# Kernel optimization log

Hardware: AMD Instinct MI355X
Metric: run time of the kernel (lower is better)

## Reference

```python
import jax, jax.numpy as jnp
import numpy as np

N_NODES = 50000
N_EDGES = 800000
NUM_FEATS = 128
HIDDEN = 256
NUM_GRAPHS = 512
BN_EPS = 1e-5


def setup_inputs() -> dict:
    key = jax.random.key(0)
    ks = jax.random.split(key, 12)
    x = jax.random.normal(ks[0], (N_NODES, NUM_FEATS), dtype=jnp.float32)
    edge_index = jax.random.randint(ks[1], (2, N_EDGES), 0, N_NODES, dtype=jnp.int64)
    batch = jnp.sort(jax.random.randint(ks[2], (N_NODES,), 0, NUM_GRAPHS, dtype=jnp.int64))
    s1 = 1.0 / np.sqrt(NUM_FEATS)
    s2 = 1.0 / np.sqrt(HIDDEN)
    return {
        "x": x,
        "edge_index": edge_index,
        "batch": batch,
        "w1a": jax.random.normal(ks[3], (NUM_FEATS, HIDDEN), dtype=jnp.float32) * s1,
        "b1a": jnp.zeros((HIDDEN,), jnp.float32),
        "w2a": jax.random.normal(ks[4], (HIDDEN, HIDDEN), dtype=jnp.float32) * s2,
        "b2a": jnp.zeros((HIDDEN,), jnp.float32),
        "ga": jnp.ones((HIDDEN,), jnp.float32),
        "ba": jnp.zeros((HIDDEN,), jnp.float32),
        "w1s": jax.random.normal(ks[5], (2, HIDDEN, HIDDEN), dtype=jnp.float32) * s2,
        "b1s": jnp.zeros((2, HIDDEN), jnp.float32),
        "w2s": jax.random.normal(ks[6], (2, HIDDEN, HIDDEN), dtype=jnp.float32) * s2,
        "b2s": jnp.zeros((2, HIDDEN), jnp.float32),
        "gs": jnp.ones((2, HIDDEN), jnp.float32),
        "bs": jnp.zeros((2, HIDDEN), jnp.float32),
    }


def _gin_layer(h, src, dst, w1, b1, w2, b2, gamma, beta):
    # GIN aggregation: (1 + eps=0) * x + sum over in-neighbors
    agg = jax.ops.segment_sum(h[src], dst, num_segments=N_NODES)
    z = h + agg
    z = jax.nn.relu(z @ w1 + b1)
    z = jax.nn.relu(z @ w2 + b2)
    # BatchNorm1d (training mode: biased batch statistics over nodes)
    mu = jnp.mean(z, axis=0)
    var = jnp.var(z, axis=0)
    return gamma * (z - mu) * jax.lax.rsqrt(var + BN_EPS) + beta


def reference(x, edge_index, batch, w1a, b1a, w2a, b2a, ga, ba,
              w1s, b1s, w2s, b2s, gs, bs):
    src, dst = edge_index[0], edge_index[1]
    h = _gin_layer(x, src, dst, w1a, b1a, w2a, b2a, ga, ba)
    for i in range(w1s.shape[0]):
        h = _gin_layer(h, src, dst, w1s[i], b1s[i], w2s[i], b2s[i], gs[i], bs[i])
    # global_mean_pool over graph ids
    sums = jax.ops.segment_sum(h, batch, num_segments=NUM_GRAPHS)
    counts = jax.ops.segment_sum(jnp.ones((h.shape[0],), h.dtype), batch,
                                 num_segments=NUM_GRAPHS)
    return sums / jnp.maximum(counts, 1.0)[:, None]
```

## Files before the change

kernel.cpp:

```cpp
#include <hip/hip_runtime.h>
#include <cstdint>
#include <cstddef>


constexpr int N_NODES  = 50000;
constexpr int N_EDGES  = 800000;
constexpr int F_IN     = 128;
constexpr int HID      = 256;
constexpr int N_GRAPHS = 512;
constexpr float BN_EPS = 1e-5f;

constexpr int SCAN_CHUNK = 4096;
constexpr int SCAN_NB    = (N_NODES + SCAN_CHUNK - 1) / SCAN_CHUNK;

typedef unsigned short u16;
typedef u16 u16x2 __attribute__((ext_vector_type(2)));
typedef u16 u16x4 __attribute__((ext_vector_type(4)));
typedef u16 u16x8 __attribute__((ext_vector_type(8)));
typedef _Float16 f16;
typedef f16 f16x8 __attribute__((ext_vector_type(8)));
typedef float f32x4 __attribute__((ext_vector_type(4)));

__device__ __forceinline__ u16 f2h(float f) {
    _Float16 h = (_Float16)f;
    return __builtin_bit_cast(u16, h);
}
__device__ __forceinline__ float h2f(u16 h) {
    return (float)__builtin_bit_cast(_Float16, h);
}

__device__ __forceinline__ void gload16(const void* g, void* l) {
    __builtin_amdgcn_global_load_lds(
        (const __attribute__((address_space(1))) uint32_t*)g,
        (__attribute__((address_space(3))) uint32_t*)l, 16, 0, 0);
}

__global__ void f2h_k(const float* __restrict__ in, u16* __restrict__ outp, int n8) {
    int i = blockIdx.x * 256 + threadIdx.x;
    if (i >= n8) return;
    float4 a = reinterpret_cast<const float4*>(in)[i * 2];
    float4 b = reinterpret_cast<const float4*>(in)[i * 2 + 1];
    u16x8 v;
    v[0] = f2h(a.x); v[1] = f2h(a.y); v[2] = f2h(a.z); v[3] = f2h(a.w);
    v[4] = f2h(b.x); v[5] = f2h(b.y); v[6] = f2h(b.z); v[7] = f2h(b.w);
    reinterpret_cast<u16x8*>(outp)[i] = v;
}

__global__ void hist_k(const int* __restrict__ dst, int* __restrict__ deg) {
    int e = blockIdx.x * 256 + threadIdx.x;
    if (e < N_EDGES) atomicAdd(&deg[dst[e]], 1);
}

__global__ void scan_part1(const int* __restrict__ in, int* __restrict__ bsum) {
    __shared__ int sm[256];
    int t = threadIdx.x;
    int base = blockIdx.x * SCAN_CHUNK + t * 16;
    int s = 0;
#pragma unroll
    for (int j = 0; j < 16; j++) { int idx = base + j; s += (idx < N_NODES) ? in[idx] : 0; }
    sm[t] = s; __syncthreads();
    for (int off = 128; off > 0; off >>= 1) {
        if (t < off) sm[t] += sm[t + off];
        __syncthreads();
    }
    if (t == 0) bsum[blockIdx.x] = sm[0];
}

__global__ void scan_tops(int* __restrict__ bsum, int* __restrict__ rowptr) {
    if (threadIdx.x == 0 && blockIdx.x == 0) {
        int acc = 0;
        for (int i = 0; i < SCAN_NB; i++) { int v = bsum[i]; bsum[i] = acc; acc += v; }
        rowptr[N_NODES] = acc;
    }
}

__global__ void scan_final(const int* __restrict__ in, const int* __restrict__ bsum,
                           int* __restrict__ rowptr, int* __restrict__ cursor) {
    __shared__ int sm[256];
    int t = threadIdx.x;
    int base = blockIdx.x * SCAN_CHUNK + t * 16;
    int loc[16]; int s = 0;
#pragma unroll
    for (int j = 0; j < 16; j++) { int idx = base + j; loc[j] = s; s += (idx < N_NODES) ? in[idx] : 0; }
    sm[t] = s; __syncthreads();
    for (int off = 1; off < 256; off <<= 1) {
        int v = (t >= off) ? sm[t - off] : 0;
        __syncthreads();
        sm[t] += v;
        __syncthreads();
    }
    int excl = sm[t] - s + bsum[blockIdx.x];
#pragma unroll
    for (int j = 0; j < 16; j++) {
        int idx = base + j;
        if (idx < N_NODES) { int rp = excl + loc[j]; rowptr[idx] = rp; cursor[idx] = rp; }
    }
}

__global__ void build_csr(const int* __restrict__ src, const int* __restrict__ dst,
                          int* __restrict__ cursor, int* __restrict__ col) {
    int e = blockIdx.x * 256 + threadIdx.x;
    if (e < N_EDGES) {
        int d = dst[e];
        int p = atomicAdd(&cursor[d], 1);
        col[p] = src[e];
    }
}

template <int F, bool FOLD>
__global__ __launch_bounds__(256) void aggregate_k(const u16* __restrict__ h,
                                                   const int* __restrict__ rowptr,
                                                   const int* __restrict__ col,
                                                   const float* __restrict__ stats,
                                                   const float* __restrict__ gamma,
                                                   const float* __restrict__ beta,
                                                   u16* __restrict__ outp) {
    int node = blockIdx.x * 4 + (threadIdx.x >> 6);
    if (node >= N_NODES) return;
    int lane = threadIdx.x & 63;
    int beg = rowptr[node], end = rowptr[node + 1];
    if constexpr (F == 256) {
        float sc[4], sh[4];
        if constexpr (FOLD) {
            int c4 = lane * 4;
#pragma unroll
            for (int i = 0; i < 4; i++) {
                float mu  = stats[c4 + i] * (1.f / N_NODES);
                float var = stats[HID + c4 + i] * (1.f / N_NODES) - mu * mu;
                float g = gamma[c4 + i] * rsqrtf(var + BN_EPS);
                sc[i] = g;
                sh[i] = beta[c4 + i] - mu * g;
            }
        }
        const u16x4* hp = reinterpret_cast<const u16x4*>(h);
        u16x4 sv = hp[(size_t)node * 64 + lane];
        float acc[4] = {h2f(sv[0]), h2f(sv[1]), h2f(sv[2]), h2f(sv[3])};
        int e = beg;
        for (; e + 4 <= end; e += 4) {
            int s0 = col[e], s1 = col[e + 1], s2 = col[e + 2], s3 = col[e + 3];
            u16x4 v0 = hp[(size_t)s0 * 64 + lane];
            u16x4 v1 = hp[(size_t)s1 * 64 + lane];
            u16x4 v2 = hp[(size_t)s2 * 64 + lane];
            u16x4 v3 = hp[(size_t)s3 * 64 + lane];
#pragma unroll
            for (int i = 0; i < 4; i++)
                acc[i] += (h2f(v0[i]) + h2f(v1[i])) + (h2f(v2[i]) + h2f(v3[i]));
        }
        for (; e < end; ++e) {
            int s = col[e];
            u16x4 v = hp[(size_t)s * 64 + lane];
#pragma unroll
            for (int i = 0; i < 4; i++) acc[i] += h2f(v[i]);
        }
        if constexpr (FOLD) {
            float m = (float)(end - beg + 1);
#pragma unroll
            for (int i = 0; i < 4; i++) acc[i] = acc[i] * sc[i] + m * sh[i];
        }
        u16x4 r;
#pragma unroll
        for (int i = 0; i < 4; i++) r[i] = f2h(acc[i]);
        reinterpret_cast<u16x4*>(outp)[(size_t)node * 64 + lane] = r;
    } else {
        const u16x2* hp = reinterpret_cast<const u16x2*>(h);
        u16x2 sv = hp[(size_t)node * 64 + lane];
        float acc[2] = {h2f(sv[0]), h2f(sv[1])};
        int e = beg;
        for (; e + 4 <= end; e += 4) {
            int s0 = col[e], s1 = col[e + 1], s2 = col[e + 2], s3 = col[e + 3];
            u16x2 v0 = hp[(size_t)s0 * 64 + lane];
            u16x2 v1 = hp[(size_t)s1 * 64 + lane];
            u16x2 v2 = hp[(size_t)s2 * 64 + lane];
            u16x2 v3 = hp[(size_t)s3 * 64 + lane];
#pragma unroll
            for (int i = 0; i < 2; i++)
                acc[i] += (h2f(v0[i]) + h2f(v1[i])) + (h2f(v2[i]) + h2f(v3[i]));
        }
        for (; e < end; ++e) {
            int s = col[e];
            u16x2 v = hp[(size_t)s * 64 + lane];
#pragma unroll
            for (int i = 0; i < 2; i++) acc[i] += h2f(v[i]);
        }
        u16x2 r;
        r[0] = f2h(acc[0]); r[1] = f2h(acc[1]);
        reinterpret_cast<u16x2*>(outp)[(size_t)node * 64 + lane] = r;
    }
}

__global__ void wconv_all(const float* __restrict__ w1a, const float* __restrict__ w2a,
                          const float* __restrict__ w1s, const float* __restrict__ w2s,
                          u16* __restrict__ th) {
    int idx = blockIdx.x * 256 + threadIdx.x;
    const float* W; int local; size_t dof;
    if (idx < 32768)       { W = w1a;         local = idx;          dof = 0; }
    else if (idx < 98304)  { W = w2a;         local = idx - 32768;  dof = 32768; }
    else if (idx < 163840) { W = w1s;         local = idx - 98304;  dof = 98304; }
    else if (idx < 229376) { W = w1s + 65536; local = idx - 163840; dof = 163840; }
    else if (idx < 294912) { W = w2s;         local = idx - 229376; dof = 229376; }
    else if (idx < 360448) { W = w2s + 65536; local = idx - 294912; dof = 294912; }
    else return;
    int n = local & 255, k = local >> 8;
    float f = W[(size_t)k * 256 + n];
    int t = k >> 5, j = (k >> 3) & 3, e = k & 7;
    int uo = j ^ ((n >> 1) & 3);
    th[dof + (size_t)t * 8192 + n * 32 + uo * 8 + e] = f2h(f);
}

template <int K, bool STATS>
__global__ __launch_bounds__(256, 2) void gemm_mfma(const u16* __restrict__ A,
                                                    const u16* __restrict__ Wth,
                                                    const float* __restrict__ bias,
                                                    u16* __restrict__ C,
                                                    float* __restrict__ stats) {
    constexpr int BM = 128, BK = 32;
    __shared__ alignas(16) u16 Ah[BM * BK];
    __shared__ alignas(16) u16 Bh[HID * BK];
    __shared__ float smsum[HID];
    __shared__ float smsq[HID];

    const int tid  = threadIdx.x;
    const int r0   = blockIdx.x * BM;
    const int lane = tid & 63, wv = tid >> 6;
    const int wm = wv >> 1, wn = wv & 1;
    const int l15 = lane & 15, kg = lane >> 4;

    int aro[2], aco[2];
#pragma unroll
    for (int p = 0; p < 2; p++) {
        int nu = wv * 128 + p * 64 + lane;
        int r = nu >> 2, us = nu & 3;
        int u = us ^ ((r >> 1) & 3);
        aro[p] = r;
        aco[p] = u * 8;
    }

    f32x4 acc[4][8];
#pragma unroll
    for (int i = 0; i < 4; i++)
#pragma unroll
        for (int j = 0; j < 8; j++) acc[i][j] = (f32x4){0.f, 0.f, 0.f, 0.f};

    for (int k0 = 0; k0 < K; k0 += BK) {
        int t = k0 >> 5;
#pragma unroll
        for (int p = 0; p < 2; p++) {
            const u16* src = A + (size_t)(r0 + aro[p]) * K + k0 + aco[p];
            gload16(src, (char*)Ah + (size_t)(wv * 2 + p) * 1024);
        }
        const char* wh = (const char*)Wth + (size_t)t * 16384 + (size_t)wv * 4096 + (size_t)lane * 16;
#pragma unroll
        for (int c = 0; c < 4; c++)
            gload16(wh + c * 1024, (char*)Bh + (size_t)wv * 4096 + c * 1024);
        __syncthreads();
        f16x8 ah[4];
#pragma unroll
        for (int mi = 0; mi < 4; mi++) {
            int r = wm * 64 + mi * 16 + l15;
            int off = r * 64 + ((kg ^ ((r >> 1) & 3)) << 4);
            ah[mi] = __builtin_bit_cast(f16x8, *reinterpret_cast<const u16x8*>((const char*)Ah + off));
        }
#pragma unroll
        for (int ni = 0; ni < 8; ni++) {
            int n = wn * 128 + ni * 16 + l15;
            int off = n * 64 + ((kg ^ ((n >> 1) & 3)) << 4);
            f16x8 bh = __builtin_bit_cast(f16x8, *reinterpret_cast<const u16x8*>((const char*)Bh + off));
#pragma unroll
            for (int mi = 0; mi < 4; mi++)
                acc[mi][ni] = __builtin_amdgcn_mfma_f32_16x16x32_f16(ah[mi], bh, acc[mi][ni], 0, 0, 0);
        }
        __syncthreads();
    }
    if constexpr (STATS) {
        smsum[tid] = 0.f;
        smsq[tid]  = 0.f;
        __syncthreads();
    }
    float bv[8];
#pragma unroll
    for (int ni = 0; ni < 8; ni++) bv[ni] = bias[wn * 128 + ni * 16 + l15];
    float ps[8] = {}, pq[8] = {};
#pragma unroll
    for (int mi = 0; mi < 4; mi++) {
        int rowb = r0 + wm * 64 + mi * 16 + kg * 4;
#pragma unroll
        for (int rr = 0; rr < 4; rr++) {
            int row = rowb + rr;
            if (row < N_NODES) {
                u16* cp = C + (size_t)row * HID + wn * 128 + l15;
#pragma unroll
                for (int ni = 0; ni < 8; ni++) {
                    float v = fmaxf(acc[mi][ni][rr] + bv[ni], 0.f);
                    cp[ni * 16] = f2h(v);
                    if constexpr (STATS) { ps[ni] += v; pq[ni] += v * v; }
                }
            }
        }
    }
    if constexpr (STATS) {
#pragma unroll
        for (int ni = 0; ni < 8; ni++) {
            int c = wn * 128 + ni * 16 + l15;
            atomicAdd(&smsum[c], ps[ni]);
            atomicAdd(&smsq[c], pq[ni]);
        }
        __syncthreads();
        atomicAdd(&stats[tid], smsum[tid]);
        atomicAdd(&stats[HID + tid], smsq[tid]);
    }
}

__device__ __forceinline__ int lowerb(const int* a, int key) {
    int lo = 0, hi = N_NODES;
    while (lo < hi) { int mid = (lo + hi) >> 1; if (a[mid] < key) lo = mid + 1; else hi = mid; }
    return lo;
}

__global__ void pool_k(const u16* __restrict__ h, const int* __restrict__ batch,
                       const float* __restrict__ stats, const float* __restrict__ gamma,
                       const float* __restrict__ beta, float* __restrict__ out) {
    __shared__ int bnd[2];
    int g = blockIdx.x;
    if (threadIdx.x == 0) bnd[0] = lowerb(batch, g);
    if (threadIdx.x == 1) bnd[1] = lowerb(batch, g + 1);
    __syncthreads();
    int lo = bnd[0], hi = bnd[1];
    int c = threadIdx.x;
    float mu  = stats[c] * (1.f / N_NODES);
    float var = stats[HID + c] * (1.f / N_NODES) - mu * mu;
    float sc = gamma[c] * rsqrtf(var + BN_EPS);
    float sh = beta[c] - mu * sc;
    float s = 0.f;
    for (int r = lo; r < hi; ++r) s += h2f(h[(size_t)r * HID + c]);
    int cnt = hi - lo;
    float v = (cnt > 0) ? (sc * (s / (float)cnt) + sh) : 0.f;
    out[(size_t)g * HID + c] = v;
}

extern "C" void kernel_launch(void* const* d_in, const int* in_sizes, int n_in,
                              void* d_out, int out_size, void* d_ws, size_t ws_size,
                              hipStream_t stream) {
    const float* x   = (const float*)d_in[0];
    const int*   ei  = (const int*)d_in[1];
    const int* batch = (const int*)d_in[2];
    const float* w1a = (const float*)d_in[3];
    const float* b1a = (const float*)d_in[4];
    const float* w2a = (const float*)d_in[5];
    const float* b2a = (const float*)d_in[6];
    const float* ga  = (const float*)d_in[7];
    const float* ba  = (const float*)d_in[8];
    const float* w1s = (const float*)d_in[9];
    const float* b1s = (const float*)d_in[10];
    const float* w2s = (const float*)d_in[11];
    const float* b2s = (const float*)d_in[12];
    const float* gs  = (const float*)d_in[13];
    const float* bs  = (const float*)d_in[14];
    const int* src = ei;
    const int* dst = ei + N_EDGES;

    char* ws = (char*)d_ws;
    size_t off = 0;
    auto alloc = [&](size_t bytes) { void* p = ws + off; off += (bytes + 255) & ~(size_t)255; return p; };
    u16* A      = (u16*)alloc(sizeof(u16) * (size_t)N_NODES * HID);
    u16* B      = (u16*)alloc(sizeof(u16) * (size_t)N_NODES * HID);
    u16* Xb     = (u16*)alloc(sizeof(u16) * (size_t)N_NODES * F_IN);
    int* rowptr = (int*)alloc(sizeof(int) * (N_NODES + 1));
    int* deg    = (int*)alloc(sizeof(int) * N_NODES);
    int* cursor = (int*)alloc(sizeof(int) * N_NODES);
    int* col    = (int*)alloc(sizeof(int) * N_EDGES);
    int* bsum   = (int*)alloc(sizeof(int) * 64);
    float* stats  = (float*)alloc(sizeof(float) * 512 * 3);
    constexpr size_t WT_TOT = 32768 + 5 * 65536;
    u16* WtH = (u16*)alloc(sizeof(u16) * WT_TOT);
    constexpr size_t o1a = 0, o2a = 32768, o1s0 = 98304, o1s1 = 163840, o2s0 = 229376, o2s1 = 294912;
    float* out    = (float*)d_out;
    (void)ws_size; (void)in_sizes; (void)n_in; (void)out_size;

    f2h_k<<<(N_NODES * F_IN / 8 + 255) / 256, 256, 0, stream>>>(x, Xb, N_NODES * F_IN / 8);
    wconv_all<<<(360448 + 255) / 256, 256, 0, stream>>>(w1a, w2a, w1s, w2s, WtH);
    hipMemsetAsync(stats, 0, sizeof(float) * 512 * 3, stream);

    hipMemsetAsync(deg, 0, sizeof(int) * N_NODES, stream);
    hist_k<<<N_EDGES / 256, 256, 0, stream>>>(dst, deg);
    scan_part1<<<SCAN_NB, 256, 0, stream>>>(deg, bsum);
    scan_tops<<<1, 64, 0, stream>>>(bsum, rowptr);
    scan_final<<<SCAN_NB, 256, 0, stream>>>(deg, bsum, rowptr, cursor);
    build_csr<<<N_EDGES / 256, 256, 0, stream>>>(src, dst, cursor, col);

    const int AGG_GRID  = (N_NODES + 3) / 4;
    const int GEMM_GRID = (N_NODES + 127) / 128;

    aggregate_k<128, false><<<AGG_GRID, 256, 0, stream>>>(Xb, rowptr, col, nullptr, nullptr, nullptr, A);
    gemm_mfma<128, false><<<GEMM_GRID, 256, 0, stream>>>(A, WtH + o1a, b1a, B, nullptr);
    gemm_mfma<256, true><<<GEMM_GRID, 256, 0, stream>>>(B, WtH + o2a, b2a, B, stats);

    aggregate_k<256, true><<<AGG_GRID, 256, 0, stream>>>(B, rowptr, col, stats, ga, ba, A);
    gemm_mfma<256, false><<<GEMM_GRID, 256, 0, stream>>>(A, WtH + o1s0, b1s, A, nullptr);
    gemm_mfma<256, true><<<GEMM_GRID, 256, 0, stream>>>(A, WtH + o2s0, b2s, A, stats + 512);

    aggregate_k<256, true><<<AGG_GRID, 256, 0, stream>>>(A, rowptr, col, stats + 512, gs, bs, B);
    gemm_mfma<256, false><<<GEMM_GRID, 256, 0, stream>>>(B, WtH + o1s1, b1s + 256, B, nullptr);
    gemm_mfma<256, true><<<GEMM_GRID, 256, 0, stream>>>(B, WtH + o2s1, b2s + 256, B, stats + 1024);

    pool_k<<<N_GRAPHS, 256, 0, stream>>>(B, batch, stats + 1024, gs + 256, bs + 256, out);
}
```

Before: 445.3 us.

## Halve GEMM row tile for more blocks and fuse prep kernels into one

The MFMA GEMM tile shrinks from 128 to 64 rows. Each of the four waves now owns a 64-column slice instead of a 2x2 warp grid, and launch bounds rise to 4 blocks per CU. This doubles the grid so work spreads more evenly across the CUs and occupancy goes up, at the cost of loading each weight tile twice as often. Separately, input fp16 conversion, weight swizzle conversion, and the deg/stats zeroing memsets are merged into one prep kernel to cut launch overhead.

```diff
diff --git a/kernel.cpp b/kernel.cpp
--- a/kernel.cpp
+++ b/kernel.cpp
@@ -35,15 +35,36 @@
         (__attribute__((address_space(3))) uint32_t*)l, 16, 0, 0);
 }
 
-__global__ void f2h_k(const float* __restrict__ in, u16* __restrict__ outp, int n8) {
-    int i = blockIdx.x * 256 + threadIdx.x;
-    if (i >= n8) return;
-    float4 a = reinterpret_cast<const float4*>(in)[i * 2];
-    float4 b = reinterpret_cast<const float4*>(in)[i * 2 + 1];
-    u16x8 v;
-    v[0] = f2h(a.x); v[1] = f2h(a.y); v[2] = f2h(a.z); v[3] = f2h(a.w);
-    v[4] = f2h(b.x); v[5] = f2h(b.y); v[6] = f2h(b.z); v[7] = f2h(b.w);
-    reinterpret_cast<u16x8*>(outp)[i] = v;
+__global__ void prep_k(const float* __restrict__ x, u16* __restrict__ Xb,
+                       const float* __restrict__ w1a, const float* __restrict__ w2a,
+                       const float* __restrict__ w1s, const float* __restrict__ w2s,
+                       u16* __restrict__ th, int* __restrict__ deg,
+                       float* __restrict__ stats) {
+    int idx = blockIdx.x * 256 + threadIdx.x;
+    {
+        float4 a = reinterpret_cast<const float4*>(x)[idx * 2];
+        float4 b = reinterpret_cast<const float4*>(x)[idx * 2 + 1];
+        u16x8 v;
+        v[0] = f2h(a.x); v[1] = f2h(a.y); v[2] = f2h(a.z); v[3] = f2h(a.w);
+        v[4] = f2h(b.x); v[5] = f2h(b.y); v[6] = f2h(b.z); v[7] = f2h(b.w);
+        reinterpret_cast<u16x8*>(Xb)[idx] = v;
+    }
+    if (idx < 360448) {
+        const float* W; int local; size_t dof;
+        if (idx < 32768)       { W = w1a;         local = idx;          dof = 0; }
+        else if (idx < 98304)  { W = w2a;         local = idx - 32768;  dof = 32768; }
+        else if (idx < 163840) { W = w1s;         local = idx - 98304;  dof = 98304; }
+        else if (idx < 229376) { W = w1s + 65536; local = idx - 163840; dof = 163840; }
+        else if (idx < 294912) { W = w2s;         local = idx - 229376; dof = 229376; }
+        else                   { W = w2s + 65536; local = idx - 294912; dof = 294912; }
+        int n = local & 255, k = local >> 8;
+        float f = W[(size_t)k * 256 + n];
+        int t = k >> 5, j = (k >> 3) & 3, e = k & 7;
+        int uo = j ^ ((n >> 1) & 3);
+        th[dof + (size_t)t * 8192 + n * 32 + uo * 8 + e] = f2h(f);
+    }
+    if (idx < N_NODES) deg[idx] = 0;
+    if (idx < 1536) stats[idx] = 0.f;
 }
 
 __global__ void hist_k(const int* __restrict__ dst, int* __restrict__ deg) {
@@ -188,32 +209,13 @@
     }
 }
 
-__global__ void wconv_all(const float* __restrict__ w1a, const float* __restrict__ w2a,
-                          const float* __restrict__ w1s, const float* __restrict__ w2s,
-                          u16* __restrict__ th) {
-    int idx = blockIdx.x * 256 + threadIdx.x;
-    const float* W; int local; size_t dof;
-    if (idx < 32768)       { W = w1a;         local = idx;          dof = 0; }
-    else if (idx < 98304)  { W = w2a;         local = idx - 32768;  dof = 32768; }
-    else if (idx < 163840) { W = w1s;         local = idx - 98304;  dof = 98304; }
-    else if (idx < 229376) { W = w1s + 65536; local = idx - 163840; dof = 163840; }
-    else if (idx < 294912) { W = w2s;         local = idx - 229376; dof = 229376; }
-    else if (idx < 360448) { W = w2s + 65536; local = idx - 294912; dof = 294912; }
-    else return;
-    int n = local & 255, k = local >> 8;
-    float f = W[(size_t)k * 256 + n];
-    int t = k >> 5, j = (k >> 3) & 3, e = k & 7;
-    int uo = j ^ ((n >> 1) & 3);
-    th[dof + (size_t)t * 8192 + n * 32 + uo * 8 + e] = f2h(f);
-}
-
 template <int K, bool STATS>
-__global__ __launch_bounds__(256, 2) void gemm_mfma(const u16* __restrict__ A,
+__global__ __launch_bounds__(256, 4) void gemm_mfma(const u16* __restrict__ A,
                                                     const u16* __restrict__ Wth,
                                                     const float* __restrict__ bias,
                                                     u16* __restrict__ C,
                                                     float* __restrict__ stats) {
-    constexpr int BM = 128, BK = 32;
+    constexpr int BM = 64, BK = 32;
     __shared__ alignas(16) u16 Ah[BM * BK];
     __shared__ alignas(16) u16 Bh[HID * BK];
     __shared__ float smsum[HID];
@@ -222,32 +224,27 @@
     const int tid  = threadIdx.x;
     const int r0   = blockIdx.x * BM;
     const int lane = tid & 63, wv = tid >> 6;
-    const int wm = wv >> 1, wn = wv & 1;
+    const int wn = wv;
     const int l15 = lane & 15, kg = lane >> 4;
 
-    int aro[2], aco[2];
-#pragma unroll
-    for (int p = 0; p < 2; p++) {
-        int nu = wv * 128 + p * 64 + lane;
+    int aro, aco;
+    {
+        int nu = wv * 64 + lane;
         int r = nu >> 2, us = nu & 3;
         int u = us ^ ((r >> 1) & 3);
-        aro[p] = r;
-        aco[p] = u * 8;
-    }
-
-    f32x4 acc[4][8];
+        aro = r;
+        aco = u * 8;
+    }
+
+    f32x4 acc[4][4];
 #pragma unroll
     for (int i = 0; i < 4; i++)
 #pragma unroll
-        for (int j = 0; j < 8; j++) acc[i][j] = (f32x4){0.f, 0.f, 0.f, 0.f};
+        for (int j = 0; j < 4; j++) acc[i][j] = (f32x4){0.f, 0.f, 0.f, 0.f};
 
     for (int k0 = 0; k0 < K; k0 += BK) {
         int t = k0 >> 5;
-#pragma unroll
-        for (int p = 0; p < 2; p++) {
-            const u16* src = A + (size_t)(r0 + aro[p]) * K + k0 + aco[p];
-            gload16(src, (char*)Ah + (size_t)(wv * 2 + p) * 1024);
-        }
+        gload16(A + (size_t)(r0 + aro) * K + k0 + aco, (char*)Ah + (size_t)wv * 1024);
         const char* wh = (const char*)Wth + (size_t)t * 16384 + (size_t)wv * 4096 + (size_t)lane * 16;
 #pragma unroll
         for (int c = 0; c < 4; c++)
@@ -256,13 +253,13 @@
         f16x8 ah[4];
 #pragma unroll
         for (int mi = 0; mi < 4; mi++) {
-            int r = wm * 64 + mi * 16 + l15;
+            int r = mi * 16 + l15;
             int off = r * 64 + ((kg ^ ((r >> 1) & 3)) << 4);
             ah[mi] = __builtin_bit_cast(f16x8, *reinterpret_cast<const u16x8*>((const char*)Ah + off));
         }
 #pragma unroll
-        for (int ni = 0; ni < 8; ni++) {
-            int n = wn * 128 + ni * 16 + l15;
+        for (int ni = 0; ni < 4; ni++) {
+            int n = wn * 64 + ni * 16 + l15;
             int off = n * 64 + ((kg ^ ((n >> 1) & 3)) << 4);
             f16x8 bh = __builtin_bit_cast(f16x8, *reinterpret_cast<const u16x8*>((const char*)Bh + off));
 #pragma unroll
@@ -276,20 +273,20 @@
         smsq[tid]  = 0.f;
         __syncthreads();
     }
-    float bv[8];
-#pragma unroll
-    for (int ni = 0; ni < 8; ni++) bv[ni] = bias[wn * 128 + ni * 16 + l15];
-    float ps[8] = {}, pq[8] = {};
+    float bv[4];
+#pragma unroll
+    for (int ni = 0; ni < 4; ni++) bv[ni] = bias[wn * 64 + ni * 16 + l15];
+    float ps[4] = {}, pq[4] = {};
 #pragma unroll
     for (int mi = 0; mi < 4; mi++) {
-        int rowb = r0 + wm * 64 + mi * 16 + kg * 4;
+        int rowb = r0 + mi * 16 + kg * 4;
 #pragma unroll
         for (int rr = 0; rr < 4; rr++) {
             int row = rowb + rr;
             if (row < N_NODES) {
-                u16* cp = C + (size_t)row * HID + wn * 128 + l15;
-#pragma unroll
-                for (int ni = 0; ni < 8; ni++) {
+                u16* cp = C + (size_t)row * HID + wn * 64 + l15;
+#pragma unroll
+                for (int ni = 0; ni < 4; ni++) {
                     float v = fmaxf(acc[mi][ni][rr] + bv[ni], 0.f);
                     cp[ni * 16] = f2h(v);
                     if constexpr (STATS) { ps[ni] += v; pq[ni] += v * v; }
@@ -299,8 +296,8 @@
     }
     if constexpr (STATS) {
 #pragma unroll
-        for (int ni = 0; ni < 8; ni++) {
-            int c = wn * 128 + ni * 16 + l15;
+        for (int ni = 0; ni < 4; ni++) {
+            int c = wn * 64 + ni * 16 + l15;
             atomicAdd(&smsum[c], ps[ni]);
             atomicAdd(&smsq[c], pq[ni]);
         }
@@ -376,11 +373,9 @@
     float* out    = (float*)d_out;
     (void)ws_size; (void)in_sizes; (void)n_in; (void)out_size;
 
-    f2h_k<<<(N_NODES * F_IN / 8 + 255) / 256, 256, 0, stream>>>(x, Xb, N_NODES * F_IN / 8);
-    wconv_all<<<(360448 + 255) / 256, 256, 0, stream>>>(w1a, w2a, w1s, w2s, WtH);
-    hipMemsetAsync(stats, 0, sizeof(float) * 512 * 3, stream);
-
-    hipMemsetAsync(deg, 0, sizeof(int) * N_NODES, stream);
+    prep_k<<<(N_NODES * F_IN / 8 + 255) / 256, 256, 0, stream>>>(
+        x, Xb, w1a, w2a, w1s, w2s, WtH, deg, stats);
+
     hist_k<<<N_EDGES / 256, 256, 0, stream>>>(dst, deg);
     scan_part1<<<SCAN_NB, 256, 0, stream>>>(deg, bsum);
     scan_tops<<<1, 64, 0, stream>>>(bsum, rowptr);
@@ -388,7 +383,7 @@
     build_csr<<<N_EDGES / 256, 256, 0, stream>>>(src, dst, cursor, col);
 
     const int AGG_GRID  = (N_NODES + 3) / 4;
-    const int GEMM_GRID = (N_NODES + 127) / 128;
+    const int GEMM_GRID = (N_NODES + 63) / 64;
 
     aggregate_k<128, false><<<AGG_GRID, 256, 0, stream>>>(Xb, rowptr, col, nullptr, nullptr, nullptr, A);
     gemm_mfma<128, false><<<GEMM_GRID, 256, 0, stream>>>(A, WtH + o1a, b1a, B, nullptr);
```

New measurement: 456.7 us. +2.5%, slower.
